# Kernel optimization log

Measured on AMD Instinct MI355X. Metric: run time of the kernel, lower is better.

The kernel has to match this reference:

```python
import jax, jax.numpy as jnp
from jax import lax
import numpy as np

B, S, E, H2, V = 128, 256, 256, 256, 50000  # batch, subword seq len, emb dim, per-direction hidden, vocab


def _make_masks(rng):
    # random subword lengths, word-start (bmask) and word-end (fmask) masks with equal counts per row
    lengths = rng.integers(S // 2, S + 1, size=B)
    pos = np.arange(S)[None, :]
    valid = pos < lengths[:, None]
    starts = (rng.random((B, S)) < 0.33) & valid
    starts[:, 0] = True
    nxt = np.concatenate([starts[:, 1:], np.zeros((B, 1), bool)], axis=1)
    fmask = valid & (nxt | (pos == lengths[:, None] - 1))
    return valid, fmask, starts


def setup_inputs():
    rng = np.random.default_rng(0)
    valid, fmask, bmask = _make_masks(rng)
    sw_ids = rng.integers(1, V, size=(B, S)) * valid  # 0 = pad
    key = jax.random.key(0)
    ks = jax.random.split(key, 8)
    se = float(np.sqrt(3.0 / E))       # random_embedding scale
    sh = float(1.0 / np.sqrt(H2))      # pytorch LSTM init scale
    u = lambda k, shape, s: jax.random.uniform(k, shape, jnp.float32, -s, s)
    return {
        "sw_ids": jnp.asarray(sw_ids, jnp.int32),
        "fmasks": jnp.asarray(fmask, jnp.int32),
        "bmasks": jnp.asarray(bmask, jnp.int32),
        "emb_W": u(ks[0], (V, E), se),
        "W_ih_f": u(ks[1], (4 * H2, E), sh),
        "W_hh_f": u(ks[2], (4 * H2, H2), sh),
        "b_f": u(ks[3], (4 * H2,), sh),
        "W_ih_b": u(ks[4], (4 * H2, E), sh),
        "W_hh_b": u(ks[5], (4 * H2, H2), sh),
        "b_b": u(ks[6], (4 * H2,), sh),
    }


def _lstm(x, mask, Wih, Whh, b):
    # x: [B,S,E]; mask: [B,S] float. Matches packed LSTM: state frozen and output
    # zeroed at padded steps (pad_packed_sequence zero-pads). Gate order i,f,g,o.
    h0 = jnp.zeros((x.shape[0], Whh.shape[1]), x.dtype)

    def step(carry, inp):
        h, c = carry
        xt, mt = inp
        g = xt @ Wih.T + h @ Whh.T + b
        i, f, gg, o = jnp.split(g, 4, axis=-1)
        c_new = jax.nn.sigmoid(f) * c + jax.nn.sigmoid(i) * jnp.tanh(gg)
        h_new = jax.nn.sigmoid(o) * jnp.tanh(c_new)
        m = mt[:, None]
        h = jnp.where(m > 0, h_new, h)
        c = jnp.where(m > 0, c_new, c)
        return (h, c), h * m

    _, ys = lax.scan(step, (h0, h0), (x.transpose(1, 0, 2), mask.T))
    return ys.transpose(1, 0, 2)  # [B,S,H2]


def _select_pad(out, mask, out_len):
    # vectorized masked_select + pad_sequence: stable-sort moves mask==1 positions
    # (in original order) to the front of the time axis, then zero beyond out_len.
    gather = jnp.argsort(1 - mask, axis=1)  # stable -> selected positions first
    sel = jnp.take_along_axis(out, gather[:, :, None], axis=1)
    word_valid = jnp.arange(out.shape[1])[None, :] < out_len[:, None]
    return sel * word_valid[:, :, None].astype(out.dtype)


def reference(sw_ids, fmasks, bmasks, emb_W, W_ih_f, W_hh_f, b_f, W_ih_b, W_hh_b, b_b):
    lengths = (sw_ids != 0).sum(axis=1)
    perm = jnp.argsort(-lengths)  # stable descending, like torch sort(descending=True)
    ids = sw_ids[perm]
    fm = fmasks[perm]
    bm = bmasks[perm]
    valid = (ids != 0).astype(emb_W.dtype)
    embeds = emb_W[ids]  # dropout is identity at eval time
    f_out = _lstm(embeds, valid, W_ih_f, W_hh_f, b_f)
    # backward direction: reverse in time (padding leads but state stays zero under mask)
    b_out = _lstm(embeds[:, ::-1], valid[:, ::-1], W_ih_b, W_hh_b, b_b)[:, ::-1]
    out_len = fm.sum(axis=1)
    f_pad = _select_pad(f_out, fm, out_len)
    b_pad = _select_pad(b_out, bm, out_len)
    perm2 = jnp.argsort(-out_len)
    out = jnp.concatenate([f_pad[perm2], b_pad[perm2]], axis=2)  # [B, S, 2*H2]
    return out, out_len[perm2]
```

## Files before the change

kernel.cpp:

```cpp
#include <hip/hip_runtime.h>
#include <hip/hip_bf16.h>
#include <hip/hip_fp16.h>
#include <math.h>
#include <stdint.h>

#define BB 128
#define SS 256
#define EE 256
#define HH 256
#define G4 1024
#define OUT_HEAD (BB*SS*2*HH)
#define SE 0.10825317547305482f
#define QX (127.0f/SE)

#define P4_HH_F 0
#define P4_HH_B 32768
#define P8_IH_F 131072
#define P8_IH_B 196608
#define SC_OFF  (1024*1024)
#define INT_OFF (1280*1024)
#define GX_OFF  (4*1024*1024)

typedef _Float16 h4v __attribute__((ext_vector_type(4)));

__device__ __forceinline__ float sigf(float x){ return 1.0f/(1.0f+__expf(-x)); }
__device__ __forceinline__ float tanhx(float x){
    float t = __expf(2.0f*x);
    return 1.0f - 2.0f/(t+1.0f);
}
__device__ __forceinline__ int dot4(uint32_t a, uint32_t b, int acc){
    return __builtin_amdgcn_sdot4((int)a, (int)b, acc, false);
}

__global__ __launch_bounds__(64) void pack8(const float* __restrict__ W,
    uint32_t* __restrict__ P8, float* __restrict__ SC){
    const int g = blockIdx.x, lane = threadIdx.x;
    float4 w4 = ((const float4*)(W + (size_t)g*EE))[lane];
    float m = fmaxf(fmaxf(fabsf(w4.x), fabsf(w4.y)), fmaxf(fabsf(w4.z), fabsf(w4.w)));
    for(int off=32; off; off>>=1) m = fmaxf(m, __shfl_xor(m, off));
    const float inv = (m > 0.f) ? 127.f/m : 0.f;
    int b0 = (int)rintf(w4.x*inv), b1 = (int)rintf(w4.y*inv);
    int b2 = (int)rintf(w4.z*inv), b3 = (int)rintf(w4.w*inv);
    uint32_t p = (uint32_t)(b0 & 0xff) | ((uint32_t)(b1 & 0xff) << 8) |
                 ((uint32_t)(b2 & 0xff) << 16) | ((uint32_t)(b3 & 0xff) << 24);
    P8[lane*G4 + g] = p;
    if(lane == 0) SC[g] = m / 127.f;
}

__global__ __launch_bounds__(64) void pack4x(const float* __restrict__ W,
    uint32_t* __restrict__ P4, float* __restrict__ SC){
    const int g = blockIdx.x, lane = threadIdx.x;
    float4 w4 = ((const float4*)(W + (size_t)g*EE))[lane];
    float m = fmaxf(fmaxf(fabsf(w4.x), fabsf(w4.y)), fmaxf(fabsf(w4.z), fabsf(w4.w)));
    for(int off=32; off; off>>=1) m = fmaxf(m, __shfl_xor(m, off));
    const float inv = (m > 0.f) ? 7.f/m : 0.f;
    int q0 = (int)rintf(w4.x*inv) + 8, q1 = (int)rintf(w4.y*inv) + 8;
    int q2 = (int)rintf(w4.z*inv) + 8, q3 = (int)rintf(w4.w*inv) + 8;
    uint32_t mypack = (uint32_t)q0 | ((uint32_t)q1 << 8) |
                      ((uint32_t)q2 << 16) | ((uint32_t)q3 << 24);
    uint32_t other = __shfl_xor(mypack, 1);
    if(!(lane & 1)) P4[(size_t)(lane>>1)*G4 + g] = mypack | (other << 4);
    if(lane == 0) SC[g] = m / 7.f;
}

__global__ void prep(const int* __restrict__ sw, const int* __restrict__ fm,
                     const int* __restrict__ bm, int* __restrict__ wsI,
                     float* __restrict__ out_tail){
    __shared__ int len_s[BB], flen_s[BB], perm_s[BB], olp_s[BB];
    int b = threadIdx.x;
    int cnt = 0, fcnt = 0;
    for(int t=0;t<SS;t++){
        cnt  += (sw[b*SS+t] != 0);
        fcnt += fm[b*SS+t];
    }
    len_s[b] = cnt; flen_s[b] = fcnt;
    __syncthreads();
    int r = 0;
    for(int b2=0;b2<BB;b2++){
        int l2 = len_s[b2];
        r += (l2 > cnt) || (l2 == cnt && b2 < b);
    }
    perm_s[r] = b;
    __syncthreads();
    int orig = perm_s[b];
    olp_s[b] = flen_s[orig];
    wsI[0*BB + b] = orig;
    wsI[1*BB + b] = len_s[orig];
    __syncthreads();
    int v = olp_s[b];
    int q = 0;
    for(int r2=0;r2<BB;r2++){
        int v2 = olp_s[r2];
        q += (v2 > v) || (v2 == v && r2 < b);
    }
    wsI[2*BB + b] = q;
    wsI[3*BB + b] = v;
    out_tail[q] = (float)v;
    int* fdst = wsI + 4*BB;
    int* bdst = fdst + BB*SS;
    int fc = 0, bc = 0;
    for(int t=0;t<SS;t++){
        int fv = fm[orig*SS+t];
        fdst[b*SS+t] = (fv && fc < v) ? (q*SS + fc) : -1;
        fc += fv;
        int bv = bm[orig*SS+t];
        bdst[b*SS+t] = (bv && bc < v) ? (q*SS + bc) : -1;
        bc += bv;
    }
}

__global__ __launch_bounds__(1024)
__attribute__((amdgpu_waves_per_eu(4,4)))
void xg32(const int* __restrict__ sw, const float* __restrict__ emb,
    const float* __restrict__ b_f, const float* __restrict__ b_b,
    const uint32_t* __restrict__ wsU, const float* __restrict__ scl,
    const int* __restrict__ wsI, _Float16* __restrict__ gx){
    __shared__ __align__(16) uint32_t xqT[64*32];
    const int tid = threadIdx.x, r = blockIdx.x, dir = blockIdx.y;
    const uint32_t* P = wsU + (dir ? P8_IH_B : P8_IH_F);
    const int gt = tid & 255;
    const int tt = tid >> 8;
    const int orig = wsI[r], L = wsI[BB + r];
    const int* ids = sw + orig*SS;
    _Float16* gxr = gx + ((size_t)(dir*BB + r))*SS*G4;
    const float* bias = dir ? b_b : b_f;
    const float* scA = scl + (2+dir)*G4;
    float bs[4], cs[4];
    #pragma unroll
    for(int g=0;g<4;g++){ bs[g] = bias[gt*4+g]; cs[g] = scA[gt*4+g]*(SE/127.f); }
    const int kq = tid & 31, dq = tid >> 5;

    for(int t0 = 0; t0 < L; t0 += 32){
        int tq = t0 + kq;
        #pragma unroll
        for(int q=0;q<2;q++){
            int d = dq + q*32;
            uint32_t pv = 0u;
            if(tq < L && d < 64){
                float4 xf = ((const float4*)(emb + (size_t)ids[tq]*EE))[d];
                int b0=(int)rintf(xf.x*QX), b1=(int)rintf(xf.y*QX);
                int b2=(int)rintf(xf.z*QX), b3=(int)rintf(xf.w*QX);
                pv = (uint32_t)(b0 & 0xff) | ((uint32_t)(b1 & 0xff) << 8) |
                     ((uint32_t)(b2 & 0xff) << 16) | ((uint32_t)(b3 & 0xff) << 24);
            }
            if(d < 64) xqT[d*32 + kq] = pv;
        }
        __syncthreads();

        int acc[4][8];
        #pragma unroll
        for(int g=0;g<4;g++)
            #pragma unroll
            for(int k=0;k<8;k++) acc[g][k] = 0;

        const uint4* xv4 = (const uint4*)xqT;
        #pragma unroll 4
        for(int j=0;j<64;j++){
            uint4 wv = *(const uint4*)&P[j*G4 + gt*4];
            uint4 xa = xv4[j*8 + tt*2];
            uint4 xb = xv4[j*8 + tt*2 + 1];
            #pragma unroll
            for(int g=0;g<4;g++){
                uint32_t w = ((const uint32_t*)&wv)[g];
                acc[g][0] = dot4(w, xa.x, acc[g][0]);
                acc[g][1] = dot4(w, xa.y, acc[g][1]);
                acc[g][2] = dot4(w, xa.z, acc[g][2]);
                acc[g][3] = dot4(w, xa.w, acc[g][3]);
                acc[g][4] = dot4(w, xb.x, acc[g][4]);
                acc[g][5] = dot4(w, xb.y, acc[g][5]);
                acc[g][6] = dot4(w, xb.z, acc[g][6]);
                acc[g][7] = dot4(w, xb.w, acc[g][7]);
            }
        }

        #pragma unroll
        for(int k=0;k<8;k++){
            int t = t0 + tt*8 + k;
            if(t < L){
                h4v hv;
                #pragma unroll
                for(int g=0;g<4;g++) hv[g] = (_Float16)(bs[g] + (float)acc[g][k]*cs[g]);
                *((h4v*)(gxr + (size_t)t*G4 + gt*4)) = hv;
            }
        }
        __syncthreads();
    }
}

__global__ __launch_bounds__(1024)
__attribute__((amdgpu_waves_per_eu(4,4)))
void rec4S(const uint32_t* __restrict__ wsU, const float* __restrict__ scl,
    const int* __restrict__ wsI, const _Float16* __restrict__ gx,
    float* __restrict__ out){
    __shared__ float gfl[G4];
    __shared__ __align__(16) int h8i[64];
    __shared__ int hsp[4];
    const int tid = threadIdx.x, r = blockIdx.x, dir = blockIdx.y;
    const uint32_t* P = wsU + (dir ? P4_HH_B : P4_HH_F);
    const float csh = scl[dir*G4 + tid] * (1.f/127.f);
    const int L = wsI[BB + r];
    const int* dstA = wsI + 4*BB + (dir ? BB*SS : 0) + r*SS;
    if(tid < 64) h8i[tid] = 0;
    if(tid < 4) hsp[tid] = 0;
    float cst = 0.f;
    const _Float16* gxr = gx + ((size_t)(dir*BB + r))*SS*G4;
    const int t0 = dir ? L-1 : 0, stp = dir ? -1 : 1;
    _Float16 gv = gxr[(size_t)t0*G4 + tid];
    __syncthreads();

    for(int s=0;s<L;s++){
        const int t = t0 + s*stp;
        const float gxv = (float)gv;
        if(s+1 < L) gv = gxr[(size_t)(t+stp)*G4 + tid];
        const int sum_h = hsp[0] + hsp[1] + hsp[2] + hsp[3];
        int acc0 = 0, acc1 = 0;
        const uint4* hp4 = (const uint4*)h8i;
        const uint32_t M = 0x0F0F0F0Fu;
        #pragma unroll
        for(int i=0;i<16;i++){
            uint32_t wa = P[(2*i  )*G4 + tid];
            uint32_t wb = P[(2*i+1)*G4 + tid];
            uint4 hh = hp4[i];
            acc0 = dot4( wa       & M, hh.x, acc0);
            acc1 = dot4((wa >> 4) & M, hh.y, acc1);
            acc0 = dot4( wb       & M, hh.z, acc0);
            acc1 = dot4((wb >> 4) & M, hh.w, acc1);
        }
        gfl[tid] = gxv + (float)(acc0 + acc1 - 8*sum_h)*csh;
        __syncthreads();
        if(tid < HH){
            float gi = gfl[tid], gf = gfl[tid+256], gz = gfl[tid+512], go = gfl[tid+768];
            float i = sigf(gi), f = sigf(gf), z = tanhx(gz), o = sigf(go);
            cst = f*cst + i*z;
            float hn = o*tanhx(cst);
            int hq = (int)rintf(hn*127.f);
            ((signed char*)h8i)[tid] = (signed char)hq;
            int sh = hq;
            for(int off=32; off; off>>=1) sh += __shfl_xor(sh, off);
            if((tid & 63) == 0) hsp[tid >> 6] = sh;
            int dst = dstA[t];
            if(dst >= 0) out[(size_t)dst*(2*HH) + dir*HH + tid] = hn;
        }
        __syncthreads();
    }
}

extern "C" void kernel_launch(void* const* d_in, const int* in_sizes, int n_in,
                              void* d_out, int out_size, void* d_ws, size_t ws_size,
                              hipStream_t stream){
    const int*   sw    = (const int*)d_in[0];
    const int*   fm    = (const int*)d_in[1];
    const int*   bm    = (const int*)d_in[2];
    const float* emb   = (const float*)d_in[3];
    const float* Wih_f = (const float*)d_in[4];
    const float* Whh_f = (const float*)d_in[5];
    const float* b_f   = (const float*)d_in[6];
    const float* Wih_b = (const float*)d_in[7];
    const float* Whh_b = (const float*)d_in[8];
    const float* b_b   = (const float*)d_in[9];
    float* out = (float*)d_out;
    uint32_t* wsU = (uint32_t*)d_ws;
    float* scl = (float*)((char*)d_ws + SC_OFF);
    int* wsI = (int*)((char*)d_ws + INT_OFF);
    _Float16* gxp = (_Float16*)((char*)d_ws + GX_OFF);

    hipMemsetAsync(d_out, 0, (size_t)out_size*4, stream);
    pack4x<<<G4, 64, 0, stream>>>(Whh_f, wsU + P4_HH_F, scl + 0*G4);
    pack4x<<<G4, 64, 0, stream>>>(Whh_b, wsU + P4_HH_B, scl + 1*G4);
    pack8<<<G4, 64, 0, stream>>>(Wih_f, wsU + P8_IH_F, scl + 2*G4);
    pack8<<<G4, 64, 0, stream>>>(Wih_b, wsU + P8_IH_B, scl + 3*G4);
    prep<<<1, BB, 0, stream>>>(sw, fm, bm, wsI, out + OUT_HEAD);
    xg32<<<dim3(BB,2), 1024, 0, stream>>>(sw, emb, b_f, b_b, wsU, scl, wsI, gxp);
    rec4S<<<dim3(BB,2), 1024, 0, stream>>>(wsU, scl, wsI, gxp, out);
}
```

Baseline: 563.8 us.

## Switch recurrent weights to int8 with half held in LDS, half streamed

Recurrent W_hh is now quantized to int8 instead of packed int4. A new pack kernel splits it: the first half is laid out in a chunked form that each recurrence block copies once into a 128KB shared-memory buffer, and the second half stays in global memory in the old strided layout. Each step reads half its weights from LDS, which should relieve the L2/global streaming that limits the sequential loop. It also drops the nibble unpacking and the per-step sum-of-h correction with its shuffle reduction. The cost is a large LDS footprint per block, which limits occupancy to one block per CU, plus an upfront 128KB copy per block.

```diff
diff --git a/kernel.cpp b/kernel.cpp
--- a/kernel.cpp
+++ b/kernel.cpp
@@ -13,12 +13,14 @@
 #define SE 0.10825317547305482f
 #define QX (127.0f/SE)
 
-#define P4_HH_F 0
-#define P4_HH_B 32768
-#define P8_IH_F 131072
-#define P8_IH_B 196608
-#define SC_OFF  (1024*1024)
-#define INT_OFF (1280*1024)
+#define P8C_HH_F 0
+#define P8C_HH_B 32768
+#define P8_HH_F  65536
+#define P8_HH_B  131072
+#define P8_IH_F  196608
+#define P8_IH_B  262144
+#define SC_OFF  1310720
+#define INT_OFF 1339392
 #define GX_OFF  (4*1024*1024)
 
 typedef _Float16 h4v __attribute__((ext_vector_type(4)));
@@ -30,6 +32,22 @@
 }
 __device__ __forceinline__ int dot4(uint32_t a, uint32_t b, int acc){
     return __builtin_amdgcn_sdot4((int)a, (int)b, acc, false);
+}
+
+__global__ __launch_bounds__(64) void pack8hy(const float* __restrict__ W,
+    uint32_t* __restrict__ P8, uint32_t* __restrict__ P8C, float* __restrict__ SC){
+    const int g = blockIdx.x, lane = threadIdx.x;
+    float4 w4 = ((const float4*)(W + (size_t)g*EE))[lane];
+    float m = fmaxf(fmaxf(fabsf(w4.x), fabsf(w4.y)), fmaxf(fabsf(w4.z), fabsf(w4.w)));
+    for(int off=32; off; off>>=1) m = fmaxf(m, __shfl_xor(m, off));
+    const float inv = (m > 0.f) ? 127.f/m : 0.f;
+    int b0 = (int)rintf(w4.x*inv), b1 = (int)rintf(w4.y*inv);
+    int b2 = (int)rintf(w4.z*inv), b3 = (int)rintf(w4.w*inv);
+    uint32_t p = (uint32_t)(b0 & 0xff) | ((uint32_t)(b1 & 0xff) << 8) |
+                 ((uint32_t)(b2 & 0xff) << 16) | ((uint32_t)(b3 & 0xff) << 24);
+    if(lane < 32) P8C[(lane >> 2)*4096 + g*4 + (lane & 3)] = p;
+    else          P8[(size_t)lane*G4 + g] = p;
+    if(lane == 0) SC[g] = m / 127.f;
 }
 
 __global__ __launch_bounds__(64) void pack8(const float* __restrict__ W,
@@ -43,24 +61,8 @@
     int b2 = (int)rintf(w4.z*inv), b3 = (int)rintf(w4.w*inv);
     uint32_t p = (uint32_t)(b0 & 0xff) | ((uint32_t)(b1 & 0xff) << 8) |
                  ((uint32_t)(b2 & 0xff) << 16) | ((uint32_t)(b3 & 0xff) << 24);
-    P8[lane*G4 + g] = p;
+    P8[(size_t)lane*G4 + g] = p;
     if(lane == 0) SC[g] = m / 127.f;
-}
-
-__global__ __launch_bounds__(64) void pack4x(const float* __restrict__ W,
-    uint32_t* __restrict__ P4, float* __restrict__ SC){
-    const int g = blockIdx.x, lane = threadIdx.x;
-    float4 w4 = ((const float4*)(W + (size_t)g*EE))[lane];
-    float m = fmaxf(fmaxf(fabsf(w4.x), fabsf(w4.y)), fmaxf(fabsf(w4.z), fabsf(w4.w)));
-    for(int off=32; off; off>>=1) m = fmaxf(m, __shfl_xor(m, off));
-    const float inv = (m > 0.f) ? 7.f/m : 0.f;
-    int q0 = (int)rintf(w4.x*inv) + 8, q1 = (int)rintf(w4.y*inv) + 8;
-    int q2 = (int)rintf(w4.z*inv) + 8, q3 = (int)rintf(w4.w*inv) + 8;
-    uint32_t mypack = (uint32_t)q0 | ((uint32_t)q1 << 8) |
-                      ((uint32_t)q2 << 16) | ((uint32_t)q3 << 24);
-    uint32_t other = __shfl_xor(mypack, 1);
-    if(!(lane & 1)) P4[(size_t)(lane>>1)*G4 + g] = mypack | (other << 4);
-    if(lane == 0) SC[g] = m / 7.f;
 }
 
 __global__ void prep(const int* __restrict__ sw, const int* __restrict__ fm,
@@ -187,21 +189,21 @@
     }
 }
 
-__global__ __launch_bounds__(1024)
-__attribute__((amdgpu_waves_per_eu(4,4)))
-void rec4S(const uint32_t* __restrict__ wsU, const float* __restrict__ scl,
-    const int* __restrict__ wsI, const _Float16* __restrict__ gx,
-    float* __restrict__ out){
+__global__ __launch_bounds__(1024,4) void rec6(const uint32_t* __restrict__ wsU,
+    const float* __restrict__ scl, const int* __restrict__ wsI,
+    const _Float16* __restrict__ gx, float* __restrict__ out){
+    __shared__ __align__(16) uint32_t WL[32768];
     __shared__ float gfl[G4];
     __shared__ __align__(16) int h8i[64];
-    __shared__ int hsp[4];
     const int tid = threadIdx.x, r = blockIdx.x, dir = blockIdx.y;
-    const uint32_t* P = wsU + (dir ? P4_HH_B : P4_HH_F);
+    const uint32_t* PC = wsU + (dir ? P8C_HH_B : P8C_HH_F);
+    const uint32_t* PS = wsU + (dir ? P8_HH_B : P8_HH_F);
+    #pragma unroll
+    for(int i=0;i<32;i++) WL[i*1024 + tid] = PC[i*1024 + tid];
     const float csh = scl[dir*G4 + tid] * (1.f/127.f);
     const int L = wsI[BB + r];
     const int* dstA = wsI + 4*BB + (dir ? BB*SS : 0) + r*SS;
     if(tid < 64) h8i[tid] = 0;
-    if(tid < 4) hsp[tid] = 0;
     float cst = 0.f;
     const _Float16* gxr = gx + ((size_t)(dir*BB + r))*SS*G4;
     const int t0 = dir ? L-1 : 0, stp = dir ? -1 : 1;
@@ -212,32 +214,37 @@
         const int t = t0 + s*stp;
         const float gxv = (float)gv;
         if(s+1 < L) gv = gxr[(size_t)(t+stp)*G4 + tid];
-        const int sum_h = hsp[0] + hsp[1] + hsp[2] + hsp[3];
         int acc0 = 0, acc1 = 0;
-        const uint4* hp4 = (const uint4*)h8i;
-        const uint32_t M = 0x0F0F0F0Fu;
-        #pragma unroll
-        for(int i=0;i<16;i++){
-            uint32_t wa = P[(2*i  )*G4 + tid];
-            uint32_t wb = P[(2*i+1)*G4 + tid];
-            uint4 hh = hp4[i];
-            acc0 = dot4( wa       & M, hh.x, acc0);
-            acc1 = dot4((wa >> 4) & M, hh.y, acc1);
-            acc0 = dot4( wb       & M, hh.z, acc0);
-            acc1 = dot4((wb >> 4) & M, hh.w, acc1);
-        }
-        gfl[tid] = gxv + (float)(acc0 + acc1 - 8*sum_h)*csh;
+        const uint4* hp = (const uint4*)h8i;
+        #pragma unroll
+        for(int ch=0;ch<8;ch++){
+            uint4 wv = *(const uint4*)&WL[ch*4096 + tid*4];
+            uint4 hv = hp[ch];
+            acc0 = dot4(wv.x, hv.x, acc0);
+            acc1 = dot4(wv.y, hv.y, acc1);
+            acc0 = dot4(wv.z, hv.z, acc0);
+            acc1 = dot4(wv.w, hv.w, acc1);
+        }
+        #pragma unroll
+        for(int i=0;i<8;i++){
+            uint32_t w0 = PS[(size_t)(32+4*i+0)*G4 + tid];
+            uint32_t w1 = PS[(size_t)(32+4*i+1)*G4 + tid];
+            uint32_t w2 = PS[(size_t)(32+4*i+2)*G4 + tid];
+            uint32_t w3 = PS[(size_t)(32+4*i+3)*G4 + tid];
+            uint4 hv = hp[8+i];
+            acc0 = dot4(w0, hv.x, acc0);
+            acc1 = dot4(w1, hv.y, acc1);
+            acc0 = dot4(w2, hv.z, acc0);
+            acc1 = dot4(w3, hv.w, acc1);
+        }
+        gfl[tid] = gxv + (float)(acc0 + acc1)*csh;
         __syncthreads();
         if(tid < HH){
             float gi = gfl[tid], gf = gfl[tid+256], gz = gfl[tid+512], go = gfl[tid+768];
             float i = sigf(gi), f = sigf(gf), z = tanhx(gz), o = sigf(go);
             cst = f*cst + i*z;
             float hn = o*tanhx(cst);
-            int hq = (int)rintf(hn*127.f);
-            ((signed char*)h8i)[tid] = (signed char)hq;
-            int sh = hq;
-            for(int off=32; off; off>>=1) sh += __shfl_xor(sh, off);
-            if((tid & 63) == 0) hsp[tid >> 6] = sh;
+            ((signed char*)h8i)[tid] = (signed char)(int)rintf(hn*127.f);
             int dst = dstA[t];
             if(dst >= 0) out[(size_t)dst*(2*HH) + dir*HH + tid] = hn;
         }
@@ -265,11 +272,11 @@
     _Float16* gxp = (_Float16*)((char*)d_ws + GX_OFF);
 
     hipMemsetAsync(d_out, 0, (size_t)out_size*4, stream);
-    pack4x<<<G4, 64, 0, stream>>>(Whh_f, wsU + P4_HH_F, scl + 0*G4);
-    pack4x<<<G4, 64, 0, stream>>>(Whh_b, wsU + P4_HH_B, scl + 1*G4);
+    pack8hy<<<G4, 64, 0, stream>>>(Whh_f, wsU + P8_HH_F, wsU + P8C_HH_F, scl + 0*G4);
+    pack8hy<<<G4, 64, 0, stream>>>(Whh_b, wsU + P8_HH_B, wsU + P8C_HH_B, scl + 1*G4);
     pack8<<<G4, 64, 0, stream>>>(Wih_f, wsU + P8_IH_F, scl + 2*G4);
     pack8<<<G4, 64, 0, stream>>>(Wih_b, wsU + P8_IH_B, scl + 3*G4);
     prep<<<1, BB, 0, stream>>>(sw, fm, bm, wsI, out + OUT_HEAD);
     xg32<<<dim3(BB,2), 1024, 0, stream>>>(sw, emb, b_f, b_b, wsU, scl, wsI, gxp);
-    rec4S<<<dim3(BB,2), 1024, 0, stream>>>(wsU, scl, wsI, gxp, out);
-}
+    rec6<<<dim3(BB,2), 1024, 0, stream>>>(wsU, scl, wsI, gxp, out);
+}
```

After: 526.1 us. 1.07x faster.
